# Optimization experiments

Hardware: AMD Instinct MI355X
Metric: run time of the kernel (lower is better)

The kernel has to match this reference:

```python
import jax, jax.numpy as jnp
import numpy as np

NY, NX = 320, 320
NT = 160
SHOTS, NSRC, NREC = 2, 8, 96
DT = 4.0e-4
DH = 4.0
PML_W = 20
MAX_VEL = 1600.0
C1, C2 = 9.0 / 8.0, -1.0 / 24.0  # 4th-order staggered-grid FD coefficients


def _profile(n, w, d0):
    d = np.zeros(n, np.float64)
    i = np.arange(n, dtype=np.float64)
    d[:w] = d0 * ((w - i[:w]) / w) ** 2
    d[n - w:] = d0 * ((i[n - w:] - (n - 1 - w)) / w) ** 2
    return d


def _pml_b():
    # PML damping profile d(x) = d0*(x/L)^2, CPML decay factor b = exp(-d*dt)
    d0 = 3.0 * MAX_VEL * np.log(1000.0) / (2.0 * PML_W * DH)
    by = np.exp(-_profile(NY, PML_W, d0) * DT).astype(np.float32)
    bx = np.exp(-_profile(NX, PML_W, d0) * DT).astype(np.float32)
    return jnp.asarray(by)[None, :, None], jnp.asarray(bx)[None, None, :]


def _edge_mask():
    # mirrors zero_edges: kill wraparound contamination at the grid border
    m = np.ones((NY, NX), np.float32)
    m[:2, :] = 0.0
    m[-2:, :] = 0.0
    m[:, :2] = 0.0
    m[:, -2:] = 0.0
    return jnp.asarray(m)


def _d(f, axis, fwd):
    # staggered 4th-order forward (D+) / backward (D-) difference along axis
    if fwd:
        return (C1 * (jnp.roll(f, -1, axis) - f)
                + C2 * (jnp.roll(f, -2, axis) - jnp.roll(f, 1, axis))) * (1.0 / DH)
    return (C1 * (f - jnp.roll(f, 1, axis))
            + C2 * (jnp.roll(f, -1, axis) - jnp.roll(f, 2, axis))) * (1.0 / DH)


def _simulate(lamb, mu, buoyancy, amps, src_loc, rec_loc, checkpoint=False):
    by, bx = _pml_b()
    mask = _edge_mask()
    lam2mu = lamb + 2.0 * mu
    bidx = jnp.arange(SHOTS)[:, None]
    sy, sx = src_loc[..., 0], src_loc[..., 1]
    ry, rx = rec_loc[..., 0], rec_loc[..., 1]
    src_buoy = buoyancy[sy, sx]  # [shot, nsrc]
    zero = jnp.zeros((SHOTS, NY, NX), lamb.dtype)
    carry0 = tuple(zero for _ in range(13))

    def step(c, amp_t):
        (vy, vx, syy, sxy, sxx,
         mvyy, mvyx, mvxy, mvxx,
         msyyy, msxyy, msxyx, msxxx) = c
        # --- velocity update (with CPML memory variables) ---
        d = _d(syy, 1, False)
        msyyy = by * msyyy + (by - 1.0) * d
        ay = d + msyyy
        d = _d(sxy, 2, True)
        msxyx = bx * msxyx + (bx - 1.0) * d
        ay = ay + d + msxyx
        vy = vy + DT * buoyancy * ay
        d = _d(sxx, 2, False)
        msxxx = bx * msxxx + (bx - 1.0) * d
        ax = d + msxxx
        d = _d(sxy, 1, True)
        msxyy = by * msxyy + (by - 1.0) * d
        ax = ax + d + msxyy
        vx = vx + DT * buoyancy * ax
        # --- inject y-oriented sources into vy ---
        vy = vy.at[bidx, sy, sx].add(DT * amp_t * src_buoy)
        vy = vy * mask
        vx = vx * mask
        # --- stress update ---
        d = _d(vy, 1, True)
        mvyy = by * mvyy + (by - 1.0) * d
        e1 = d + mvyy
        d = _d(vx, 2, False)
        mvxx = bx * mvxx + (bx - 1.0) * d
        e2 = d + mvxx
        syy = (syy + DT * (lam2mu * e1 + lamb * e2)) * mask
        sxx = (sxx + DT * (lam2mu * e2 + lamb * e1)) * mask
        d = _d(vy, 2, True)
        mvyx = bx * mvyx + (bx - 1.0) * d
        g = d + mvyx
        d = _d(vx, 1, False)
        mvxy = by * mvxy + (by - 1.0) * d
        g = g + d + mvxy
        sxy = (sxy + DT * mu * g) * mask
        rec = vy[bidx, ry, rx]  # [shot, nrec]
        return (vy, vx, syy, sxy, sxx, mvyy, mvyx, mvxy, mvxx,
                msyyy, msxyy, msxyx, msxxx), rec

    f = jax.checkpoint(step) if checkpoint else step
    _, recs = jax.lax.scan(f, carry0, jnp.transpose(amps, (2, 0, 1)))
    # velocity receivers sampled at t+/-1/2 -> average adjacent time samples
    recs = (recs[1:] + recs[:-1]) * 0.5  # [nt-1, shot, nrec]
    return jnp.transpose(recs, (1, 2, 0))  # [shot, nrec, nt-1]


def setup_inputs() -> dict:
    key = jax.random.key(0)
    k1, k2, k3, k4, k5, k6 = jax.random.split(key, 6)
    u_l = jax.random.uniform(k1, (NY, NX), jnp.float32)
    u_m = jax.random.uniform(k2, (NY, NX), jnp.float32)
    u_b = jax.random.uniform(k3, (NY, NX), jnp.float32)
    lamb = (2.0e9 * (1.0 + 0.2 * u_l)).astype(jnp.float32)
    mu = (0.8e9 * (1.0 + 0.2 * u_m)).astype(jnp.float32)
    buoyancy = (1.0 / (1800.0 + 400.0 * u_b)).astype(jnp.float32)
    source_amplitudes_y = jax.random.normal(k4, (SHOTS, NSRC, NT), jnp.float32)
    source_locations_y = jax.random.randint(k5, (SHOTS, NSRC, 2), PML_W + 4, NY - PML_W - 4)
    receiver_locations_y = jax.random.randint(k6, (SHOTS, NREC, 2), PML_W + 4, NY - PML_W - 4)
    return {
        'lamb': lamb, 'mu': mu, 'buoyancy': buoyancy,
        'source_amplitudes_y': source_amplitudes_y,
        'source_locations_y': source_locations_y,
        'receiver_locations_y': receiver_locations_y,
    }


def reference(lamb, mu, buoyancy, source_amplitudes_y,
              source_locations_y, receiver_locations_y):
    return _simulate(lamb, mu, buoyancy, source_amplitudes_y,
                     source_locations_y, receiver_locations_y)
```

## Files before the change

kernel.cpp:

```cpp
#include <hip/hip_runtime.h>
#include <math.h>

constexpr int NY_ = 320, NX_ = 320, NT_ = 160, SHOTS_ = 2, NSRC_ = 8, NREC_ = 96;
constexpr float DT_  = 4.0e-4f;
constexpr float C1_  = 9.0f / 8.0f;
constexpr float C2_  = -1.0f / 24.0f;
constexpr float IDH_ = 0.25f;
constexpr int NSTRIP_ = 40;
constexpr int NBLK_   = SHOTS_ * NSTRIP_;
constexpr int SLOT_    = 6 * NX_;
constexpr int VS_OFF_  = 0;
constexpr int SS_OFF_  = VS_OFF_ + 2 * SHOTS_ * NSTRIP_ * SLOT_;
constexpr int REC_OFF_ = SS_OFF_ + 2 * SHOTS_ * NSTRIP_ * SLOT_;
constexpr int GF_OFF_  = REC_OFF_ + SHOTS_ * NREC_ * NT_;
constexpr int WS_WORDS_ = GF_OFF_ + 8 * NBLK_ + 64;

__device__ __forceinline__ float cld(const float* p) {
    return __hip_atomic_load(p, __ATOMIC_RELAXED, __HIP_MEMORY_SCOPE_AGENT);
}
__device__ __forceinline__ void cst(float* p, float v) {
    __hip_atomic_store(p, v, __ATOMIC_RELAXED, __HIP_MEMORY_SCOPE_AGENT);
}
__device__ __forceinline__ unsigned cldu(const unsigned* p) {
    return __hip_atomic_load(p, __ATOMIC_RELAXED, __HIP_MEMORY_SCOPE_AGENT);
}
__device__ __forceinline__ void cstu(unsigned* p, unsigned v) {
    __hip_atomic_store(p, v, __ATOMIC_RELAXED, __HIP_MEMORY_SCOPE_AGENT);
}
__device__ __forceinline__ void lwait(const unsigned* f, unsigned tgt) {
    while (__hip_atomic_load(f, __ATOMIC_ACQUIRE, __HIP_MEMORY_SCOPE_WORKGROUP) < tgt) {}
}
__device__ __forceinline__ void lpost(unsigned* f, unsigned v) {
    __hip_atomic_store(f, v, __ATOMIC_RELEASE, __HIP_MEMORY_SCOPE_WORKGROUP);
}
__device__ __forceinline__ void gwait2(const unsigned* a, const unsigned* b, unsigned tgt) {
    while (cldu(a) < tgt || cldu(b) < tgt) __builtin_amdgcn_s_sleep(1);
    asm volatile("" ::: "memory");
}
__device__ __forceinline__ float shtap(float cur, float adj, int lane, int dx) {
    int idx = (lane + dx) & 63;
    float a = __shfl(cur, idx, 64);
    float b = __shfl(adj, idx, 64);
    return ((unsigned)(lane + dx) < 64u) ? a : b;
}

__global__ void init_kernel(float* __restrict__ ws) {
    for (int i = blockIdx.x * 256 + threadIdx.x; i < WS_WORDS_; i += gridDim.x * 256)
        ws[i] = 0.0f;
}

__global__ __launch_bounds__(512, 2)
void elastic_kernel(const float* __restrict__ lamb, const float* __restrict__ mu,
                    const float* __restrict__ buoy, const float* __restrict__ amps,
                    const int* __restrict__ src_loc, const int* __restrict__ rec_loc,
                    float* __restrict__ out, float* __restrict__ ws)
{
    __shared__ float Lsyy[12][NX_], Lsxy[12][NX_], Lvy[12][NX_], Lvx[12][NX_];
    __shared__ unsigned vF[8], sF[8], hF[4];

    const int tid = threadIdx.x, lane = tid & 63, w = tid >> 6;
    const int bid = blockIdx.x, s = bid / NSTRIP_, j = bid % NSTRIP_;
    const int r0 = j * 8, gy = r0 + w, yi = w + 2;
    const int sj = s * NSTRIP_ + j;
    unsigned* gV = (unsigned*)(ws + GF_OFF_);
    unsigned* gS = gV + 4 * NBLK_;

    const double d0 = 3.0 * 1600.0 * log(1000.0) / (2.0 * 20.0 * 4.0);
    double py = 0.0;
    if (gy < 20)             { double u = (20.0 - gy) / 20.0;           py = u * u; }
    else if (gy >= NY_ - 20) { double u = (gy - (NY_ - 1 - 20)) / 20.0; py = u * u; }
    const float by = (float)exp(-d0 * py * 4.0e-4);
    const float bym1 = by - 1.0f;

    float bx[5], bxm1[5], mk[5], la[5], muv[5], bu[5], l2m[5];
    #pragma unroll
    for (int k = 0; k < 5; ++k) {
        int c = 64 * k + lane;
        double px = 0.0;
        if (c < 20)             { double u = (20.0 - c) / 20.0;           px = u * u; }
        else if (c >= NX_ - 20) { double u = (c - (NX_ - 1 - 20)) / 20.0; px = u * u; }
        bx[k] = (float)exp(-d0 * px * 4.0e-4);
        bxm1[k] = bx[k] - 1.0f;
        mk[k] = (gy < 2 || gy >= NY_ - 2 || c < 2 || c >= NX_ - 2) ? 0.0f : 1.0f;
        la[k]  = lamb[gy * NX_ + c];
        muv[k] = mu[gy * NX_ + c];
        bu[k]  = buoy[gy * NX_ + c];
        l2m[k] = la[k] + 2.0f * muv[k];
    }
    unsigned long long sm = 0ull;
    for (int js = 0; js < NSRC_; ++js) {
        int sy = src_loc[(s * NSRC_ + js) * 2 + 0];
        int sx = src_loc[(s * NSRC_ + js) * 2 + 1];
        if (sy == gy && (sx & 63) == lane) sm |= 1ull << (8 * (sx >> 6) + js);
    }
    int nrec = 0, recid[8], reck[8];
    for (int r = 0; r < NREC_; ++r) {
        int ry = rec_loc[(s * NREC_ + r) * 2 + 0];
        int rx = rec_loc[(s * NREC_ + r) * 2 + 1];
        if (ry == gy && (rx & 63) == lane && nrec < 8) { recid[nrec] = r; reck[nrec] = rx >> 6; ++nrec; }
    }
    float* recbase = ws + REC_OFF_;

    for (int i = tid; i < 12 * NX_; i += 512) {
        ((float*)Lsyy)[i] = 0.f; ((float*)Lsxy)[i] = 0.f;
        ((float*)Lvy)[i]  = 0.f; ((float*)Lvx)[i]  = 0.f;
    }
    if (tid < 8) { vF[tid] = 0u; sF[tid] = 0u; }
    if (tid < 4) hF[tid] = 0u;
    __syncthreads();

    float vy[5] = {}, vx[5] = {}, syy[5] = {}, sxy[5] = {}, sxx[5] = {};
    float msyyy[5] = {}, msxyy[5] = {}, msxyx[5] = {}, msxxx[5] = {};
    float mvyy[5] = {}, mvyx[5] = {}, mvxy[5] = {}, mvxx[5] = {};

    for (int t = 0; t < NT_; ++t) {
        const unsigned ut = (unsigned)t;
        const int pi = (t + 1) & 1, po = t & 1;

        if (w == 0) {
            if (j > 0) {
                lwait(&vF[1], ut);
                gwait2(&gS[2 * NBLK_ + (sj - 1)], &gS[3 * NBLK_ + (sj - 1)], ut);
                const float* B = ws + SS_OFF_ + ((pi * SHOTS_ + s) * NSTRIP_ + (j - 1)) * SLOT_;
                #pragma unroll
                for (int k = 0; k < 5; ++k) {
                    int c = 64 * k + lane;
                    float a = cld(B + 3 * NX_ + c), b = cld(B + 4 * NX_ + c), e = cld(B + 5 * NX_ + c);
                    Lsyy[0][c] = a; Lsyy[1][c] = b; Lsxy[1][c] = e;
                }
            }
            lpost(&hF[0], ut + 1u);
        } else if (w == 7) {
            if (j < NSTRIP_ - 1) {
                lwait(&vF[6], ut);
                gwait2(&gS[0 * NBLK_ + (sj + 1)], &gS[1 * NBLK_ + (sj + 1)], ut);
                const float* B = ws + SS_OFF_ + ((pi * SHOTS_ + s) * NSTRIP_ + (j + 1)) * SLOT_;
                #pragma unroll
                for (int k = 0; k < 5; ++k) {
                    int c = 64 * k + lane;
                    float a = cld(B + 0 * NX_ + c), b = cld(B + 1 * NX_ + c), e = cld(B + 2 * NX_ + c);
                    Lsyy[10][c] = a; Lsxy[10][c] = b; Lsxy[11][c] = e;
                }
            }
            lpost(&hF[1], ut + 1u);
        }
        if (w == 1) lwait(&hF[0], ut + 1u);
        if (w == 6) lwait(&hF[1], ut + 1u);
        if (w >= 2) lwait(&sF[w - 2], ut);
        if (w >= 1) lwait(&sF[w - 1], ut);
        if (w <= 6) lwait(&sF[w + 1], ut);
        if (w <= 5) lwait(&sF[w + 2], ut);

        #pragma unroll
        for (int k = 0; k < 5; ++k) {
            const int c = 64 * k + lane;
            const float sxyP = (k < 4) ? sxy[k + 1] : 0.0f;
            const float sxyM = (k > 0) ? sxy[k - 1] : 0.0f;
            const float sxxP = (k < 4) ? sxx[k + 1] : 0.0f;
            const float sxxM = (k > 0) ? sxx[k - 1] : 0.0f;
            float d, ay, ax;
            d = (C1_ * (syy[k] - Lsyy[yi - 1][c]) + C2_ * (Lsyy[yi + 1][c] - Lsyy[yi - 2][c])) * IDH_;
            msyyy[k] = by * msyyy[k] + bym1 * d;
            ay = d + msyyy[k];
            d = (C1_ * (shtap(sxy[k], sxyP, lane, 1) - sxy[k])
               + C2_ * (shtap(sxy[k], sxyP, lane, 2) - shtap(sxy[k], sxyM, lane, -1))) * IDH_;
            msxyx[k] = bx[k] * msxyx[k] + bxm1[k] * d;
            ay = ay + d + msxyx[k];
            vy[k] = vy[k] + DT_ * bu[k] * ay;
            d = (C1_ * (sxx[k] - shtap(sxx[k], sxxM, lane, -1))
               + C2_ * (shtap(sxx[k], sxxP, lane, 1) - shtap(sxx[k], sxxM, lane, -2))) * IDH_;
            msxxx[k] = bx[k] * msxxx[k] + bxm1[k] * d;
            ax = d + msxxx[k];
            d = (C1_ * (Lsxy[yi + 1][c] - sxy[k]) + C2_ * (Lsxy[yi + 2][c] - Lsxy[yi - 1][c])) * IDH_;
            msxyy[k] = by * msxyy[k] + bym1 * d;
            ax = ax + d + msxyy[k];
            vx[k] = vx[k] + DT_ * bu[k] * ax;
            unsigned m = (unsigned)(sm >> (8 * k)) & 0xFFu;
            if (m) {
                for (int js = 0; js < NSRC_; ++js)
                    if (m & (1u << js)) vy[k] += DT_ * amps[(s * NSRC_ + js) * NT_ + t] * bu[k];
            }
            vy[k] *= mk[k]; vx[k] *= mk[k];
            Lvy[yi][c] = vy[k]; Lvx[yi][c] = vx[k];
        }
        lpost(&vF[w], ut + 1u);
        for (int i = 0; i < nrec; ++i)
            recbase[(s * NREC_ + recid[i]) * NT_ + t] = vy[reck[i]];

        if (w == 0 || w == 1 || w == 6 || w == 7) {
            float* P = ws + VS_OFF_ + ((po * SHOTS_ + s) * NSTRIP_ + j) * SLOT_;
            #pragma unroll
            for (int k = 0; k < 5; ++k) {
                int c = 64 * k + lane;
                if (w == 0) { cst(P + 0 * NX_ + c, vy[k]); cst(P + 1 * NX_ + c, vx[k]); }
                else if (w == 1) cst(P + 2 * NX_ + c, vy[k]);
                else if (w == 6) cst(P + 3 * NX_ + c, vx[k]);
                else { cst(P + 4 * NX_ + c, vy[k]); cst(P + 5 * NX_ + c, vx[k]); }
            }
            asm volatile("s_waitcnt vmcnt(0)" ::: "memory");
            const int role = (w == 0) ? 0 : (w == 1) ? 1 : (w == 6) ? 2 : 3;
            cstu(&gV[role * NBLK_ + sj], ut + 1u);
        }

        if (w == 0) {
            if (j > 0) {
                lwait(&sF[1], ut);
                gwait2(&gV[2 * NBLK_ + (sj - 1)], &gV[3 * NBLK_ + (sj - 1)], ut + 1u);
                const float* B = ws + VS_OFF_ + ((po * SHOTS_ + s) * NSTRIP_ + (j - 1)) * SLOT_;
                #pragma unroll
                for (int k = 0; k < 5; ++k) {
                    int c = 64 * k + lane;
                    float a = cld(B + 3 * NX_ + c), b = cld(B + 4 * NX_ + c), e = cld(B + 5 * NX_ + c);
                    Lvx[0][c] = a; Lvy[1][c] = b; Lvx[1][c] = e;
                }
            }
            lpost(&hF[2], ut + 1u);
        } else if (w == 7) {
            if (j < NSTRIP_ - 1) {
                lwait(&sF[6], ut);
                gwait2(&gV[0 * NBLK_ + (sj + 1)], &gV[1 * NBLK_ + (sj + 1)], ut + 1u);
                const float* B = ws + VS_OFF_ + ((po * SHOTS_ + s) * NSTRIP_ + (j + 1)) * SLOT_;
                #pragma unroll
                for (int k = 0; k < 5; ++k) {
                    int c = 64 * k + lane;
                    float a = cld(B + 0 * NX_ + c), b = cld(B + 1 * NX_ + c), e = cld(B + 2 * NX_ + c);
                    Lvy[10][c] = a; Lvx[10][c] = b; Lvy[11][c] = e;
                }
            }
            lpost(&hF[3], ut + 1u);
        }
        if (w == 1) lwait(&hF[2], ut + 1u);
        if (w == 6) lwait(&hF[3], ut + 1u);
        if (w >= 2) lwait(&vF[w - 2], ut + 1u);
        if (w >= 1) lwait(&vF[w - 1], ut + 1u);
        if (w <= 6) lwait(&vF[w + 1], ut + 1u);
        if (w <= 5) lwait(&vF[w + 2], ut + 1u);

        #pragma unroll
        for (int k = 0; k < 5; ++k) {
            const int c = 64 * k + lane;
            const float vyP = (k < 4) ? vy[k + 1] : 0.0f;
            const float vyM = (k > 0) ? vy[k - 1] : 0.0f;
            const float vxP = (k < 4) ? vx[k + 1] : 0.0f;
            const float vxM = (k > 0) ? vx[k - 1] : 0.0f;
            float d, e1, e2, g;
            d = (C1_ * (Lvy[yi + 1][c] - vy[k]) + C2_ * (Lvy[yi + 2][c] - Lvy[yi - 1][c])) * IDH_;
            mvyy[k] = by * mvyy[k] + bym1 * d;
            e1 = d + mvyy[k];
            d = (C1_ * (vx[k] - shtap(vx[k], vxM, lane, -1))
               + C2_ * (shtap(vx[k], vxP, lane, 1) - shtap(vx[k], vxM, lane, -2))) * IDH_;
            mvxx[k] = bx[k] * mvxx[k] + bxm1[k] * d;
            e2 = d + mvxx[k];
            syy[k] = (syy[k] + DT_ * (l2m[k] * e1 + la[k] * e2)) * mk[k];
            sxx[k] = (sxx[k] + DT_ * (l2m[k] * e2 + la[k] * e1)) * mk[k];
            d = (C1_ * (shtap(vy[k], vyP, lane, 1) - vy[k])
               + C2_ * (shtap(vy[k], vyP, lane, 2) - shtap(vy[k], vyM, lane, -1))) * IDH_;
            mvyx[k] = bx[k] * mvyx[k] + bxm1[k] * d;
            g = d + mvyx[k];
            d = (C1_ * (vx[k] - Lvx[yi - 1][c]) + C2_ * (Lvx[yi + 1][c] - Lvx[yi - 2][c])) * IDH_;
            mvxy[k] = by * mvxy[k] + bym1 * d;
            g = g + d + mvxy[k];
            sxy[k] = (sxy[k] + DT_ * muv[k] * g) * mk[k];
            Lsyy[yi][c] = syy[k]; Lsxy[yi][c] = sxy[k];
        }
        lpost(&sF[w], ut + 1u);

        if (w == 0 || w == 1 || w == 6 || w == 7) {
            float* P = ws + SS_OFF_ + ((po * SHOTS_ + s) * NSTRIP_ + j) * SLOT_;
            #pragma unroll
            for (int k = 0; k < 5; ++k) {
                int c = 64 * k + lane;
                if (w == 0) { cst(P + 0 * NX_ + c, syy[k]); cst(P + 1 * NX_ + c, sxy[k]); }
                else if (w == 1) cst(P + 2 * NX_ + c, sxy[k]);
                else if (w == 6) cst(P + 3 * NX_ + c, syy[k]);
                else { cst(P + 4 * NX_ + c, syy[k]); cst(P + 5 * NX_ + c, sxy[k]); }
            }
            asm volatile("s_waitcnt vmcnt(0)" ::: "memory");
            const int role = (w == 0) ? 0 : (w == 1) ? 1 : (w == 6) ? 2 : 3;
            cstu(&gS[role * NBLK_ + sj], ut + 1u);
        }
    }

    for (int i = 0; i < nrec; ++i) {
        const float* rp = recbase + (s * NREC_ + recid[i]) * NT_;
        float* op = out + (s * NREC_ + recid[i]) * (NT_ - 1);
        for (int t = 0; t < NT_ - 1; ++t) op[t] = 0.5f * (rp[t] + rp[t + 1]);
    }
}

extern "C" void kernel_launch(void* const* d_in, const int* in_sizes, int n_in,
                              void* d_out, int out_size, void* d_ws, size_t ws_size,
                              hipStream_t stream)
{
    const float* lamb = (const float*)d_in[0];
    const float* mu   = (const float*)d_in[1];
    const float* buoy = (const float*)d_in[2];
    const float* amps = (const float*)d_in[3];
    const int*   src  = (const int*)d_in[4];
    const int*   recl = (const int*)d_in[5];
    float* out = (float*)d_out;
    float* ws  = (float*)d_ws;

    init_kernel<<<dim3(512), dim3(256), 0, stream>>>(ws);
    elastic_kernel<<<dim3(NBLK_), dim3(512), 0, stream>>>(lamb, mu, buoy, amps, src, recl, out, ws);
}
```

Before: 1.475 ms.

## Let boundary warps load halos directly into registers with per-row flags

Warps 0/1/6/7 now each fetch the neighbour-strip halo rows they need straight from global memory into registers, using per-row flags. Previously warp 0/7 staged them into padded LDS rows and signalled warps 1/6 through extra local flags. Halo writes are skipped at the domain edges and the double-buffered exchange slots are replaced by a single slot per strip. This shortens the inter-warp dependency chain and cuts LDS traffic. The single-buffered slots rely on flag ordering to avoid overwrite races.

```diff
diff --git a/kernel.cpp b/kernel.cpp
--- a/kernel.cpp
+++ b/kernel.cpp
@@ -8,12 +8,9 @@
 constexpr float IDH_ = 0.25f;
 constexpr int NSTRIP_ = 40;
 constexpr int NBLK_   = SHOTS_ * NSTRIP_;
-constexpr int SLOT_    = 6 * NX_;
-constexpr int VS_OFF_  = 0;
-constexpr int SS_OFF_  = VS_OFF_ + 2 * SHOTS_ * NSTRIP_ * SLOT_;
-constexpr int REC_OFF_ = SS_OFF_ + 2 * SHOTS_ * NSTRIP_ * SLOT_;
-constexpr int GF_OFF_  = REC_OFF_ + SHOTS_ * NREC_ * NT_;
-constexpr int WS_WORDS_ = GF_OFF_ + 8 * NBLK_ + 64;
+constexpr int FLG_OFF_ = NBLK_ * 12 * NX_;
+constexpr int REC_OFF_ = FLG_OFF_ + NBLK_ * 16;
+constexpr int WS_WORDS_ = REC_OFF_ + SHOTS_ * NREC_ * NT_ + 64;
 
 __device__ __forceinline__ float cld(const float* p) {
     return __hip_atomic_load(p, __ATOMIC_RELAXED, __HIP_MEMORY_SCOPE_AGENT);
@@ -33,7 +30,11 @@
 __device__ __forceinline__ void lpost(unsigned* f, unsigned v) {
     __hip_atomic_store(f, v, __ATOMIC_RELEASE, __HIP_MEMORY_SCOPE_WORKGROUP);
 }
-__device__ __forceinline__ void gwait2(const unsigned* a, const unsigned* b, unsigned tgt) {
+__device__ __forceinline__ void gpoll1(const unsigned* a, unsigned tgt) {
+    while (cldu(a) < tgt) __builtin_amdgcn_s_sleep(1);
+    asm volatile("" ::: "memory");
+}
+__device__ __forceinline__ void gpoll2(const unsigned* a, const unsigned* b, unsigned tgt) {
     while (cldu(a) < tgt || cldu(b) < tgt) __builtin_amdgcn_s_sleep(1);
     asm volatile("" ::: "memory");
 }
@@ -55,15 +56,17 @@
                     const int* __restrict__ src_loc, const int* __restrict__ rec_loc,
                     float* __restrict__ out, float* __restrict__ ws)
 {
-    __shared__ float Lsyy[12][NX_], Lsxy[12][NX_], Lvy[12][NX_], Lvx[12][NX_];
-    __shared__ unsigned vF[8], sF[8], hF[4];
+    __shared__ float Lvy[8][NX_], Lvx[8][NX_], Lsyy[8][NX_], Lsxy[8][NX_];
+    __shared__ unsigned vF[8], sF[8];
 
     const int tid = threadIdx.x, lane = tid & 63, w = tid >> 6;
     const int bid = blockIdx.x, s = bid / NSTRIP_, j = bid % NSTRIP_;
-    const int r0 = j * 8, gy = r0 + w, yi = w + 2;
-    const int sj = s * NSTRIP_ + j;
-    unsigned* gV = (unsigned*)(ws + GF_OFF_);
-    unsigned* gS = gV + 4 * NBLK_;
+    const int r0 = j * 8, gy = r0 + w, sj = bid;
+    const int wm1 = (w >= 1) ? w - 1 : 0, wm2 = (w >= 2) ? w - 2 : 0;
+    const int wp1 = (w <= 6) ? w + 1 : 7, wp2 = (w <= 5) ? w + 2 : 7;
+    float* SL = ws;
+    unsigned* FL = (unsigned*)(ws + FLG_OFF_);
+    float* recbase = ws + REC_OFF_;
 
     const double d0 = 3.0 * 1600.0 * log(1000.0) / (2.0 * 20.0 * 4.0);
     double py = 0.0;
@@ -90,8 +93,8 @@
     unsigned long long sm = 0ull;
     for (int js = 0; js < NSRC_; ++js) {
         int sy = src_loc[(s * NSRC_ + js) * 2 + 0];
-        int sx = src_loc[(s * NSRC_ + js) * 2 + 1];
-        if (sy == gy && (sx & 63) == lane) sm |= 1ull << (8 * (sx >> 6) + js);
+        int sxc = src_loc[(s * NSRC_ + js) * 2 + 1];
+        if (sy == gy && (sxc & 63) == lane) sm |= 1ull << (8 * (sxc >> 6) + js);
     }
     int nrec = 0, recid[8], reck[8];
     for (int r = 0; r < NREC_; ++r) {
@@ -99,53 +102,51 @@
         int rx = rec_loc[(s * NREC_ + r) * 2 + 1];
         if (ry == gy && (rx & 63) == lane && nrec < 8) { recid[nrec] = r; reck[nrec] = rx >> 6; ++nrec; }
     }
-    float* recbase = ws + REC_OFF_;
-
-    for (int i = tid; i < 12 * NX_; i += 512) {
+
+    for (int i = tid; i < 8 * NX_; i += 512) {
+        ((float*)Lvy)[i] = 0.f; ((float*)Lvx)[i] = 0.f;
         ((float*)Lsyy)[i] = 0.f; ((float*)Lsxy)[i] = 0.f;
-        ((float*)Lvy)[i]  = 0.f; ((float*)Lvx)[i]  = 0.f;
     }
     if (tid < 8) { vF[tid] = 0u; sF[tid] = 0u; }
-    if (tid < 4) hF[tid] = 0u;
     __syncthreads();
 
     float vy[5] = {}, vx[5] = {}, syy[5] = {}, sxy[5] = {}, sxx[5] = {};
     float msyyy[5] = {}, msxyy[5] = {}, msxyx[5] = {}, msxxx[5] = {};
     float mvyy[5] = {}, mvyx[5] = {}, mvxy[5] = {}, mvxx[5] = {};
 
+    const bool hasB = (j > 0), hasT = (j < NSTRIP_ - 1);
+
     for (int t = 0; t < NT_; ++t) {
         const unsigned ut = (unsigned)t;
-        const int pi = (t + 1) & 1, po = t & 1;
-
-        if (w == 0) {
-            if (j > 0) {
-                lwait(&vF[1], ut);
-                gwait2(&gS[2 * NBLK_ + (sj - 1)], &gS[3 * NBLK_ + (sj - 1)], ut);
-                const float* B = ws + SS_OFF_ + ((pi * SHOTS_ + s) * NSTRIP_ + (j - 1)) * SLOT_;
-                #pragma unroll
-                for (int k = 0; k < 5; ++k) {
-                    int c = 64 * k + lane;
-                    float a = cld(B + 3 * NX_ + c), b = cld(B + 4 * NX_ + c), e = cld(B + 5 * NX_ + c);
-                    Lsyy[0][c] = a; Lsyy[1][c] = b; Lsxy[1][c] = e;
-                }
-            }
-            lpost(&hF[0], ut + 1u);
-        } else if (w == 7) {
-            if (j < NSTRIP_ - 1) {
-                lwait(&vF[6], ut);
-                gwait2(&gS[0 * NBLK_ + (sj + 1)], &gS[1 * NBLK_ + (sj + 1)], ut);
-                const float* B = ws + SS_OFF_ + ((pi * SHOTS_ + s) * NSTRIP_ + (j + 1)) * SLOT_;
-                #pragma unroll
-                for (int k = 0; k < 5; ++k) {
-                    int c = 64 * k + lane;
-                    float a = cld(B + 0 * NX_ + c), b = cld(B + 1 * NX_ + c), e = cld(B + 2 * NX_ + c);
-                    Lsyy[10][c] = a; Lsxy[10][c] = b; Lsxy[11][c] = e;
-                }
-            }
-            lpost(&hF[1], ut + 1u);
-        }
-        if (w == 1) lwait(&hF[0], ut + 1u);
-        if (w == 6) lwait(&hF[1], ut + 1u);
+
+        float hA[5] = {}, hB[5] = {}, hC[5] = {};
+        if (w == 0 && hasB) {
+            gpoll2(&FL[(sj - 1) * 16 + 6], &FL[(sj - 1) * 16 + 7], ut);
+            const float* B = SL + (sj - 1) * 12 * NX_;
+            #pragma unroll
+            for (int k = 0; k < 5; ++k) { int c = 64 * k + lane;
+                hA[k] = cld(B + 10 * NX_ + c);
+                hB[k] = cld(B + 9  * NX_ + c);
+                hC[k] = cld(B + 11 * NX_ + c); }
+        } else if (w == 1 && hasB) {
+            gpoll1(&FL[(sj - 1) * 16 + 7], ut);
+            const float* B = SL + (sj - 1) * 12 * NX_;
+            #pragma unroll
+            for (int k = 0; k < 5; ++k) hA[k] = cld(B + 10 * NX_ + 64 * k + lane);
+        } else if (w == 6 && hasT) {
+            gpoll1(&FL[(sj + 1) * 16 + 4], ut);
+            const float* B = SL + (sj + 1) * 12 * NX_;
+            #pragma unroll
+            for (int k = 0; k < 5; ++k) hA[k] = cld(B + 7 * NX_ + 64 * k + lane);
+        } else if (w == 7 && hasT) {
+            gpoll2(&FL[(sj + 1) * 16 + 4], &FL[(sj + 1) * 16 + 5], ut);
+            const float* B = SL + (sj + 1) * 12 * NX_;
+            #pragma unroll
+            for (int k = 0; k < 5; ++k) { int c = 64 * k + lane;
+                hA[k] = cld(B + 6 * NX_ + c);
+                hB[k] = cld(B + 7 * NX_ + c);
+                hC[k] = cld(B + 8 * NX_ + c); }
+        }
         if (w >= 2) lwait(&sF[w - 2], ut);
         if (w >= 1) lwait(&sF[w - 1], ut);
         if (w <= 6) lwait(&sF[w + 1], ut);
@@ -158,8 +159,14 @@
             const float sxyM = (k > 0) ? sxy[k - 1] : 0.0f;
             const float sxxP = (k < 4) ? sxx[k + 1] : 0.0f;
             const float sxxM = (k > 0) ? sxx[k - 1] : 0.0f;
+            const float syy_m1 = (w >= 1) ? Lsyy[wm1][c] : hA[k];
+            const float syy_p1 = (w <= 6) ? Lsyy[wp1][c] : hA[k];
+            const float syy_m2 = (w >= 2) ? Lsyy[wm2][c] : ((w == 1) ? hA[k] : hB[k]);
+            const float sxy_m1 = (w >= 1) ? Lsxy[wm1][c] : hC[k];
+            const float sxy_p1 = (w <= 6) ? Lsxy[wp1][c] : hB[k];
+            const float sxy_p2 = (w <= 5) ? Lsxy[wp2][c] : ((w == 6) ? hA[k] : hC[k]);
             float d, ay, ax;
-            d = (C1_ * (syy[k] - Lsyy[yi - 1][c]) + C2_ * (Lsyy[yi + 1][c] - Lsyy[yi - 2][c])) * IDH_;
+            d = (C1_ * (syy[k] - syy_m1) + C2_ * (syy_p1 - syy_m2)) * IDH_;
             msyyy[k] = by * msyyy[k] + bym1 * d;
             ay = d + msyyy[k];
             d = (C1_ * (shtap(sxy[k], sxyP, lane, 1) - sxy[k])
@@ -171,7 +178,7 @@
                + C2_ * (shtap(sxx[k], sxxP, lane, 1) - shtap(sxx[k], sxxM, lane, -2))) * IDH_;
             msxxx[k] = bx[k] * msxxx[k] + bxm1[k] * d;
             ax = d + msxxx[k];
-            d = (C1_ * (Lsxy[yi + 1][c] - sxy[k]) + C2_ * (Lsxy[yi + 2][c] - Lsxy[yi - 1][c])) * IDH_;
+            d = (C1_ * (sxy_p1 - sxy[k]) + C2_ * (sxy_p2 - sxy_m1)) * IDH_;
             msxyy[k] = by * msxyy[k] + bym1 * d;
             ax = ax + d + msxyy[k];
             vx[k] = vx[k] + DT_ * bu[k] * ax;
@@ -181,56 +188,69 @@
                     if (m & (1u << js)) vy[k] += DT_ * amps[(s * NSRC_ + js) * NT_ + t] * bu[k];
             }
             vy[k] *= mk[k]; vx[k] *= mk[k];
-            Lvy[yi][c] = vy[k]; Lvx[yi][c] = vx[k];
+            Lvy[w][c] = vy[k]; Lvx[w][c] = vx[k];
         }
         lpost(&vF[w], ut + 1u);
         for (int i = 0; i < nrec; ++i)
             recbase[(s * NREC_ + recid[i]) * NT_ + t] = vy[reck[i]];
 
-        if (w == 0 || w == 1 || w == 6 || w == 7) {
-            float* P = ws + VS_OFF_ + ((po * SHOTS_ + s) * NSTRIP_ + j) * SLOT_;
-            #pragma unroll
-            for (int k = 0; k < 5; ++k) {
-                int c = 64 * k + lane;
-                if (w == 0) { cst(P + 0 * NX_ + c, vy[k]); cst(P + 1 * NX_ + c, vx[k]); }
-                else if (w == 1) cst(P + 2 * NX_ + c, vy[k]);
-                else if (w == 6) cst(P + 3 * NX_ + c, vx[k]);
-                else { cst(P + 4 * NX_ + c, vy[k]); cst(P + 5 * NX_ + c, vx[k]); }
-            }
-            asm volatile("s_waitcnt vmcnt(0)" ::: "memory");
-            const int role = (w == 0) ? 0 : (w == 1) ? 1 : (w == 6) ? 2 : 3;
-            cstu(&gV[role * NBLK_ + sj], ut + 1u);
-        }
-
-        if (w == 0) {
-            if (j > 0) {
-                lwait(&sF[1], ut);
-                gwait2(&gV[2 * NBLK_ + (sj - 1)], &gV[3 * NBLK_ + (sj - 1)], ut + 1u);
-                const float* B = ws + VS_OFF_ + ((po * SHOTS_ + s) * NSTRIP_ + (j - 1)) * SLOT_;
-                #pragma unroll
-                for (int k = 0; k < 5; ++k) {
-                    int c = 64 * k + lane;
-                    float a = cld(B + 3 * NX_ + c), b = cld(B + 4 * NX_ + c), e = cld(B + 5 * NX_ + c);
-                    Lvx[0][c] = a; Lvy[1][c] = b; Lvx[1][c] = e;
-                }
-            }
-            lpost(&hF[2], ut + 1u);
-        } else if (w == 7) {
-            if (j < NSTRIP_ - 1) {
-                lwait(&sF[6], ut);
-                gwait2(&gV[0 * NBLK_ + (sj + 1)], &gV[1 * NBLK_ + (sj + 1)], ut + 1u);
-                const float* B = ws + VS_OFF_ + ((po * SHOTS_ + s) * NSTRIP_ + (j + 1)) * SLOT_;
-                #pragma unroll
-                for (int k = 0; k < 5; ++k) {
-                    int c = 64 * k + lane;
-                    float a = cld(B + 0 * NX_ + c), b = cld(B + 1 * NX_ + c), e = cld(B + 2 * NX_ + c);
-                    Lvy[10][c] = a; Lvx[10][c] = b; Lvy[11][c] = e;
-                }
-            }
-            lpost(&hF[3], ut + 1u);
-        }
-        if (w == 1) lwait(&hF[2], ut + 1u);
-        if (w == 6) lwait(&hF[3], ut + 1u);
+        if (w == 0 && hasB) {
+            float* P = SL + sj * 12 * NX_;
+            #pragma unroll
+            for (int k = 0; k < 5; ++k) { int c = 64 * k + lane;
+                cst(P + 0 * NX_ + c, vy[k]); cst(P + 1 * NX_ + c, vx[k]); }
+            asm volatile("s_waitcnt vmcnt(0)" ::: "memory");
+            cstu(&FL[sj * 16 + 0], ut + 1u);
+        } else if (w == 1 && hasB) {
+            float* P = SL + sj * 12 * NX_;
+            #pragma unroll
+            for (int k = 0; k < 5; ++k) cst(P + 2 * NX_ + 64 * k + lane, vy[k]);
+            asm volatile("s_waitcnt vmcnt(0)" ::: "memory");
+            cstu(&FL[sj * 16 + 1], ut + 1u);
+        } else if (w == 6 && hasT) {
+            float* P = SL + sj * 12 * NX_;
+            #pragma unroll
+            for (int k = 0; k < 5; ++k) cst(P + 3 * NX_ + 64 * k + lane, vx[k]);
+            asm volatile("s_waitcnt vmcnt(0)" ::: "memory");
+            cstu(&FL[sj * 16 + 2], ut + 1u);
+        } else if (w == 7 && hasT) {
+            float* P = SL + sj * 12 * NX_;
+            #pragma unroll
+            for (int k = 0; k < 5; ++k) { int c = 64 * k + lane;
+                cst(P + 4 * NX_ + c, vy[k]); cst(P + 5 * NX_ + c, vx[k]); }
+            asm volatile("s_waitcnt vmcnt(0)" ::: "memory");
+            cstu(&FL[sj * 16 + 3], ut + 1u);
+        }
+
+        #pragma unroll
+        for (int k = 0; k < 5; ++k) { hA[k] = 0.f; hB[k] = 0.f; hC[k] = 0.f; }
+        if (w == 0 && hasB) {
+            gpoll2(&FL[(sj - 1) * 16 + 2], &FL[(sj - 1) * 16 + 3], ut + 1u);
+            const float* B = SL + (sj - 1) * 12 * NX_;
+            #pragma unroll
+            for (int k = 0; k < 5; ++k) { int c = 64 * k + lane;
+                hA[k] = cld(B + 4 * NX_ + c);
+                hB[k] = cld(B + 5 * NX_ + c);
+                hC[k] = cld(B + 3 * NX_ + c); }
+        } else if (w == 1 && hasB) {
+            gpoll1(&FL[(sj - 1) * 16 + 3], ut + 1u);
+            const float* B = SL + (sj - 1) * 12 * NX_;
+            #pragma unroll
+            for (int k = 0; k < 5; ++k) hA[k] = cld(B + 5 * NX_ + 64 * k + lane);
+        } else if (w == 6 && hasT) {
+            gpoll1(&FL[(sj + 1) * 16 + 0], ut + 1u);
+            const float* B = SL + (sj + 1) * 12 * NX_;
+            #pragma unroll
+            for (int k = 0; k < 5; ++k) hA[k] = cld(B + 0 * NX_ + 64 * k + lane);
+        } else if (w == 7 && hasT) {
+            gpoll2(&FL[(sj + 1) * 16 + 0], &FL[(sj + 1) * 16 + 1], ut + 1u);
+            const float* B = SL + (sj + 1) * 12 * NX_;
+            #pragma unroll
+            for (int k = 0; k < 5; ++k) { int c = 64 * k + lane;
+                hA[k] = cld(B + 0 * NX_ + c);
+                hB[k] = cld(B + 2 * NX_ + c);
+                hC[k] = cld(B + 1 * NX_ + c); }
+        }
         if (w >= 2) lwait(&vF[w - 2], ut + 1u);
         if (w >= 1) lwait(&vF[w - 1], ut + 1u);
         if (w <= 6) lwait(&vF[w + 1], ut + 1u);
@@ -243,8 +263,14 @@
             const float vyM = (k > 0) ? vy[k - 1] : 0.0f;
             const float vxP = (k < 4) ? vx[k + 1] : 0.0f;
             const float vxM = (k > 0) ? vx[k - 1] : 0.0f;
+            const float vy_p1 = (w <= 6) ? Lvy[wp1][c] : hA[k];
+            const float vy_p2 = (w <= 5) ? Lvy[wp2][c] : ((w == 6) ? hA[k] : hB[k]);
+            const float vy_m1 = (w >= 1) ? Lvy[wm1][c] : hA[k];
+            const float vx_m1 = (w >= 1) ? Lvx[wm1][c] : hB[k];
+            const float vx_m2 = (w >= 2) ? Lvx[wm2][c] : ((w == 1) ? hA[k] : hC[k]);
+            const float vx_p1 = (w <= 6) ? Lvx[wp1][c] : hC[k];
             float d, e1, e2, g;
-            d = (C1_ * (Lvy[yi + 1][c] - vy[k]) + C2_ * (Lvy[yi + 2][c] - Lvy[yi - 1][c])) * IDH_;
+            d = (C1_ * (vy_p1 - vy[k]) + C2_ * (vy_p2 - vy_m1)) * IDH_;
             mvyy[k] = by * mvyy[k] + bym1 * d;
             e1 = d + mvyy[k];
             d = (C1_ * (vx[k] - shtap(vx[k], vxM, lane, -1))
@@ -257,27 +283,40 @@
                + C2_ * (shtap(vy[k], vyP, lane, 2) - shtap(vy[k], vyM, lane, -1))) * IDH_;
             mvyx[k] = bx[k] * mvyx[k] + bxm1[k] * d;
             g = d + mvyx[k];
-            d = (C1_ * (vx[k] - Lvx[yi - 1][c]) + C2_ * (Lvx[yi + 1][c] - Lvx[yi - 2][c])) * IDH_;
+            d = (C1_ * (vx[k] - vx_m1) + C2_ * (vx_p1 - vx_m2)) * IDH_;
             mvxy[k] = by * mvxy[k] + bym1 * d;
             g = g + d + mvxy[k];
             sxy[k] = (sxy[k] + DT_ * muv[k] * g) * mk[k];
-            Lsyy[yi][c] = syy[k]; Lsxy[yi][c] = sxy[k];
+            Lsyy[w][c] = syy[k]; Lsxy[w][c] = sxy[k];
         }
         lpost(&sF[w], ut + 1u);
 
-        if (w == 0 || w == 1 || w == 6 || w == 7) {
-            float* P = ws + SS_OFF_ + ((po * SHOTS_ + s) * NSTRIP_ + j) * SLOT_;
-            #pragma unroll
-            for (int k = 0; k < 5; ++k) {
-                int c = 64 * k + lane;
-                if (w == 0) { cst(P + 0 * NX_ + c, syy[k]); cst(P + 1 * NX_ + c, sxy[k]); }
-                else if (w == 1) cst(P + 2 * NX_ + c, sxy[k]);
-                else if (w == 6) cst(P + 3 * NX_ + c, syy[k]);
-                else { cst(P + 4 * NX_ + c, syy[k]); cst(P + 5 * NX_ + c, sxy[k]); }
-            }
-            asm volatile("s_waitcnt vmcnt(0)" ::: "memory");
-            const int role = (w == 0) ? 0 : (w == 1) ? 1 : (w == 6) ? 2 : 3;
-            cstu(&gS[role * NBLK_ + sj], ut + 1u);
+        if (w == 0 && hasB) {
+            float* P = SL + sj * 12 * NX_;
+            #pragma unroll
+            for (int k = 0; k < 5; ++k) { int c = 64 * k + lane;
+                cst(P + 6 * NX_ + c, syy[k]); cst(P + 7 * NX_ + c, sxy[k]); }
+            asm volatile("s_waitcnt vmcnt(0)" ::: "memory");
+            cstu(&FL[sj * 16 + 4], ut + 1u);
+        } else if (w == 1 && hasB) {
+            float* P = SL + sj * 12 * NX_;
+            #pragma unroll
+            for (int k = 0; k < 5; ++k) cst(P + 8 * NX_ + 64 * k + lane, sxy[k]);
+            asm volatile("s_waitcnt vmcnt(0)" ::: "memory");
+            cstu(&FL[sj * 16 + 5], ut + 1u);
+        } else if (w == 6 && hasT) {
+            float* P = SL + sj * 12 * NX_;
+            #pragma unroll
+            for (int k = 0; k < 5; ++k) cst(P + 9 * NX_ + 64 * k + lane, syy[k]);
+            asm volatile("s_waitcnt vmcnt(0)" ::: "memory");
+            cstu(&FL[sj * 16 + 6], ut + 1u);
+        } else if (w == 7 && hasT) {
+            float* P = SL + sj * 12 * NX_;
+            #pragma unroll
+            for (int k = 0; k < 5; ++k) { int c = 64 * k + lane;
+                cst(P + 10 * NX_ + c, syy[k]); cst(P + 11 * NX_ + c, sxy[k]); }
+            asm volatile("s_waitcnt vmcnt(0)" ::: "memory");
+            cstu(&FL[sj * 16 + 7], ut + 1u);
         }
     }
 
```

Result: slower. 4.492 ms (+204.6%).
